# Optimization experiments

Measured on AMD Instinct MI355X. Metric: run time of the kernel, lower is better.

Reference implementation:

```python
import jax, jax.numpy as jnp
import numpy as np


def setup_inputs() -> dict:
    B, N, D, M = 512, 128, 768, 32  # bags, num_class, embed_dim, max bag size
    rng = np.random.default_rng(0)
    sizes = rng.integers(8, 25, size=B)  # variable bag sizes in [8, 24], all <= M
    offsets = np.concatenate([[0], np.cumsum(sizes)]).astype(np.int32)
    nsum = int(offsets[-1])
    scope = np.stack([offsets[:-1], offsets[1:]], axis=1)  # (B, 2) [start, end)

    key = jax.random.key(0)
    k1, k2, k3 = jax.random.split(key, 3)
    rep = jax.random.normal(k1, (nsum, D), dtype=jnp.float32)
    fc_weight = jax.random.normal(k2, (N, D), dtype=jnp.float32) * 0.02
    fc_bias = jax.random.normal(k3, (N,), dtype=jnp.float32) * 0.02
    return {
        "rep": rep,
        "fc_weight": fc_weight,
        "fc_bias": fc_bias,
        "scope": jnp.asarray(scope),
        "max_bag": M,
    }


def reference(rep, fc_weight, fc_bias, scope, max_bag):
    """IntraBagAttention forward (train=False, bag_size=0 branch), ragged bags
    rewritten as padded/masked dense ops.

    rep:       (nsum, D) sentence-encoder outputs
    fc_weight: (N, D), fc_bias: (N,)
    scope:     (B, 2) int [start, end) per bag; max_bag: static int pad bound
    returns:   (B, N) per-relation bag scores
    """
    nsum = rep.shape[0]
    starts = scope[:, 0]
    sizes = scope[:, 1] - scope[:, 0]
    pos = jnp.arange(max_bag)
    idx = jnp.clip(starts[:, None] + pos[None, :], 0, nsum - 1)  # (B, M)
    valid = pos[None, :] < sizes[:, None]                        # (B, M)
    bag = rep[idx]                                               # (B, M, D)

    # att_score = rep @ fc.weight.data.T ; .data => no grad through this use
    w_att = jax.lax.stop_gradient(fc_weight)
    att = jnp.einsum('bmd,nd->bnm', bag, w_att)                  # (B, N, M)
    att = jnp.where(valid[:, None, :], att, -jnp.inf)
    sm = jax.nn.softmax(att, axis=-1)                            # per-bag softmax over sentences

    # weighted segment sum: one attended rep per relation per bag
    rfer = jnp.einsum('bnm,bmd->bnd', sm, bag)                   # (B, N, D)

    # fc(rep_for_each_rel) -> (B, N, N); softmax over classes; take diagonal
    full = jnp.einsum('bnd,kd->bnk', rfer, fc_weight) + fc_bias  # (B, N, N)
    probs = jax.nn.softmax(full, axis=-1)
    return jnp.diagonal(probs, axis1=1, axis2=2)                 # (B, N)
```

## Files before the change

### kernel.cpp

```cpp
#include <hip/hip_runtime.h>
#include <math.h>

#define B_BAGS 512
#define N_REL  128
#define D_DIM  768

typedef __attribute__((ext_vector_type(8))) short  bf16x8;
typedef __attribute__((ext_vector_type(4))) float  f32x4;

__device__ inline unsigned pack_hi(float f0, float f1) {
    return __builtin_amdgcn_perm(__float_as_uint(f1), __float_as_uint(f0), 0x07060302u);
}
__device__ inline float trunc_res(float f) {
    return f - __uint_as_float(__float_as_uint(f) & 0xFFFF0000u);
}

__global__ void build_bfrag(const float* __restrict__ W, unsigned* __restrict__ Bfrag) {
    int flat = blockIdx.x * 256 + threadIdx.x;
    int lane = flat & 63;
    int tile = (flat >> 6) & 7;
    int s    = flat >> 9;
    int n  = tile * 16 + (lane & 15);
    int k0 = s * 32 + (lane >> 4) * 8;
    const float* src = &W[n * D_DIM + k0];
    float f[8];
    #pragma unroll
    for (int j = 0; j < 8; ++j) f[j] = src[j];
    unsigned hi[4], lo[4];
    #pragma unroll
    for (int q = 0; q < 4; ++q) {
        hi[q] = pack_hi(f[2*q], f[2*q+1]);
        lo[q] = pack_hi(trunc_res(f[2*q]), trunc_res(f[2*q+1]));
    }
    unsigned base = (unsigned)(((s * 8 + tile) * 2) * 64 + lane) * 4;
    *(uint4*)&Bfrag[base]          = make_uint4(hi[0], hi[1], hi[2], hi[3]);
    *(uint4*)&Bfrag[base + 64 * 4] = make_uint4(lo[0], lo[1], lo[2], lo[3]);
}

__global__ __launch_bounds__(512, 4) void bag_fused(
    const float*          __restrict__ rep,
    const unsigned short* __restrict__ Bfrag,
    const float*          __restrict__ bias,
    const int*            __restrict__ scope,
    float*                __restrict__ out,
    int nsum)
{
    __shared__ f32x4    Gpart[2][2][8][64];
    __shared__ unsigned Gfrag[8 * 2 * 64 * 4];
    __shared__ unsigned SMfrag[8 * 2 * 64 * 4];

    const int t = threadIdx.x;
    const int b = blockIdx.x;
    const int start = scope[2 * b];
    const int size  = scope[2 * b + 1] - start;

    const int wv   = t >> 6;
    const int lane = t & 63;
    const int nl15 = lane & 15;
    const int lg   = lane >> 4;
    const int h    = wv >> 2;
    const int q    = wv & 3;

    const float* rpA[2];
    #pragma unroll
    for (int mt = 0; mt < 2; ++mt) {
        int row = start + mt * 16 + nl15;
        row = (row > nsum - 1) ? (nsum - 1) : row;
        rpA[mt] = &rep[(size_t)row * D_DIM + h * 384 + lg * 8];
    }

    f32x4 acc[2][2][2];
    #pragma unroll
    for (int mt = 0; mt < 2; ++mt)
        #pragma unroll
        for (int ntl = 0; ntl < 2; ++ntl) {
            acc[mt][ntl][0] = f32x4{0.f, 0.f, 0.f, 0.f};
            acc[mt][ntl][1] = f32x4{0.f, 0.f, 0.f, 0.f};
        }

    float4 cr[2][2];
    uint4  cbh[2], cbl[2];
    #pragma unroll
    for (int mt = 0; mt < 2; ++mt) {
        cr[mt][0] = *(const float4*)&rpA[mt][0];
        cr[mt][1] = *(const float4*)&rpA[mt][4];
    }
    #pragma unroll
    for (int ntl = 0; ntl < 2; ++ntl) {
        const int tid8 = (h * 12) * 8 + q * 2 + ntl;
        cbh[ntl] = *(const uint4*)&Bfrag[((size_t)(tid8 * 2 + 0) * 64 + lane) * 8];
        cbl[ntl] = *(const uint4*)&Bfrag[((size_t)(tid8 * 2 + 1) * 64 + lane) * 8];
    }

    #pragma unroll
    for (int s = 0; s < 12; ++s) {
        float4 nr[2][2];
        uint4  nbh[2], nbl[2];
        if (s < 11) {
            #pragma unroll
            for (int mt = 0; mt < 2; ++mt) {
                nr[mt][0] = *(const float4*)&rpA[mt][(s + 1) * 32];
                nr[mt][1] = *(const float4*)&rpA[mt][(s + 1) * 32 + 4];
            }
            #pragma unroll
            for (int ntl = 0; ntl < 2; ++ntl) {
                const int tid8 = (h * 12 + s + 1) * 8 + q * 2 + ntl;
                nbh[ntl] = *(const uint4*)&Bfrag[((size_t)(tid8 * 2 + 0) * 64 + lane) * 8];
                nbl[ntl] = *(const uint4*)&Bfrag[((size_t)(tid8 * 2 + 1) * 64 + lane) * 8];
            }
        }

        union { unsigned u[4]; bf16x8 v; } ah[2], al[2];
        #pragma unroll
        for (int mt = 0; mt < 2; ++mt) {
            const float4 v0 = cr[mt][0];
            const float4 v1 = cr[mt][1];
            ah[mt].u[0] = pack_hi(v0.x, v0.y);
            ah[mt].u[1] = pack_hi(v0.z, v0.w);
            ah[mt].u[2] = pack_hi(v1.x, v1.y);
            ah[mt].u[3] = pack_hi(v1.z, v1.w);
            al[mt].u[0] = pack_hi(trunc_res(v0.x), trunc_res(v0.y));
            al[mt].u[1] = pack_hi(trunc_res(v0.z), trunc_res(v0.w));
            al[mt].u[2] = pack_hi(trunc_res(v1.x), trunc_res(v1.y));
            al[mt].u[3] = pack_hi(trunc_res(v1.z), trunc_res(v1.w));
        }
        #pragma unroll
        for (int ntl = 0; ntl < 2; ++ntl) {
            union { uint4 u; bf16x8 v; } bh, bl;
            bh.u = cbh[ntl];
            bl.u = cbl[ntl];
            #pragma unroll
            for (int mt = 0; mt < 2; ++mt) {
                acc[mt][ntl][0] = __builtin_amdgcn_mfma_f32_16x16x32_bf16(ah[mt].v, bh.v, acc[mt][ntl][0], 0, 0, 0);
                acc[mt][ntl][1] = __builtin_amdgcn_mfma_f32_16x16x32_bf16(ah[mt].v, bl.v, acc[mt][ntl][1], 0, 0, 0);
                acc[mt][ntl][1] = __builtin_amdgcn_mfma_f32_16x16x32_bf16(al[mt].v, bh.v, acc[mt][ntl][1], 0, 0, 0);
            }
        }

        if (s < 11) {
            #pragma unroll
            for (int mt = 0; mt < 2; ++mt) { cr[mt][0] = nr[mt][0]; cr[mt][1] = nr[mt][1]; }
            #pragma unroll
            for (int ntl = 0; ntl < 2; ++ntl) { cbh[ntl] = nbh[ntl]; cbl[ntl] = nbl[ntl]; }
        }
    }

    #pragma unroll
    for (int mt = 0; mt < 2; ++mt)
        #pragma unroll
        for (int ntl = 0; ntl < 2; ++ntl)
            Gpart[h][mt][q * 2 + ntl][lane] = acc[mt][ntl][0] + acc[mt][ntl][1];
    __syncthreads();

    const int T = wv;
    float gv[2][4], smv[2][4];
    #pragma unroll
    for (int mt = 0; mt < 2; ++mt) {
        const f32x4 p0 = Gpart[0][mt][T][lane];
        const f32x4 p1 = Gpart[1][mt][T][lane];
        #pragma unroll
        for (int r = 0; r < 4; ++r) gv[mt][r] = p0[r] + p1[r];
    }

    float vmax = -INFINITY;
    #pragma unroll
    for (int mt = 0; mt < 2; ++mt)
        #pragma unroll
        for (int r = 0; r < 4; ++r) {
            const int m = mt * 16 + lg * 4 + r;
            if (m < size) vmax = fmaxf(vmax, gv[mt][r]);
        }
    vmax = fmaxf(vmax, __shfl_xor(vmax, 16));
    vmax = fmaxf(vmax, __shfl_xor(vmax, 32));

    float ssum = 0.f;
    #pragma unroll
    for (int mt = 0; mt < 2; ++mt)
        #pragma unroll
        for (int r = 0; r < 4; ++r) {
            const int m = mt * 16 + lg * 4 + r;
            float e = (m < size) ? __expf(gv[mt][r] - vmax) : 0.f;
            smv[mt][r] = e;
            ssum += e;
        }
    ssum += __shfl_xor(ssum, 16);
    ssum += __shfl_xor(ssum, 32);
    const float inv = 1.f / ssum;
    #pragma unroll
    for (int mt = 0; mt < 2; ++mt)
        #pragma unroll
        for (int r = 0; r < 4; ++r) smv[mt][r] *= inv;

    #pragma unroll
    for (int mt = 0; mt < 2; ++mt)
        #pragma unroll
        for (int rp = 0; rp < 4; rp += 2) {
            const int m     = mt * 16 + lg * 4 + rp;
            const int lane2 = (m >> 3) * 16 + nl15;
            const int word  = (m >> 1) & 3;
            const int ihi = ((T * 2 + 0) * 64 + lane2) * 4 + word;
            const int ilo = ((T * 2 + 1) * 64 + lane2) * 4 + word;
            Gfrag[ihi]  = pack_hi(gv[mt][rp], gv[mt][rp + 1]);
            Gfrag[ilo]  = pack_hi(trunc_res(gv[mt][rp]), trunc_res(gv[mt][rp + 1]));
            SMfrag[ihi] = pack_hi(smv[mt][rp], smv[mt][rp + 1]);
            SMfrag[ilo] = pack_hi(trunc_res(smv[mt][rp]), trunc_res(smv[mt][rp + 1]));
        }
    __syncthreads();

    float bias_r[8];
    #pragma unroll
    for (int ct = 0; ct < 8; ++ct) bias_r[ct] = bias[ct * 16 + nl15];

    f32x4 facc[8];
    #pragma unroll
    for (int ct = 0; ct < 8; ++ct) facc[ct] = f32x4{0.f, 0.f, 0.f, 0.f};

    const bf16x8 ah2 = *(const bf16x8*)&SMfrag[((T * 2 + 0) * 64 + lane) * 4];
    const bf16x8 al2 = *(const bf16x8*)&SMfrag[((T * 2 + 1) * 64 + lane) * 4];
    #pragma unroll
    for (int ct = 0; ct < 8; ++ct) {
        const bf16x8 bh = *(const bf16x8*)&Gfrag[((ct * 2 + 0) * 64 + lane) * 4];
        const bf16x8 bl = *(const bf16x8*)&Gfrag[((ct * 2 + 1) * 64 + lane) * 4];
        facc[ct] = __builtin_amdgcn_mfma_f32_16x16x32_bf16(ah2, bh, facc[ct], 0, 0, 0);
        facc[ct] = __builtin_amdgcn_mfma_f32_16x16x32_bf16(ah2, bl, facc[ct], 0, 0, 0);
        facc[ct] = __builtin_amdgcn_mfma_f32_16x16x32_bf16(al2, bh, facc[ct], 0, 0, 0);
    }

    #pragma unroll
    for (int r = 0; r < 4; ++r) {
        float s[8];
        #pragma unroll
        for (int ct = 0; ct < 8; ++ct) s[ct] = facc[ct][r] + bias_r[ct];

        float mx = s[0];
        #pragma unroll
        for (int ct = 1; ct < 8; ++ct) mx = fmaxf(mx, s[ct]);
        mx = fmaxf(mx, __shfl_xor(mx, 1));
        mx = fmaxf(mx, __shfl_xor(mx, 2));
        mx = fmaxf(mx, __shfl_xor(mx, 4));
        mx = fmaxf(mx, __shfl_xor(mx, 8));

        float l = 0.f;
        #pragma unroll
        for (int ct = 0; ct < 8; ++ct) l += __expf(s[ct] - mx);
        l += __shfl_xor(l, 1);
        l += __shfl_xor(l, 2);
        l += __shfl_xor(l, 4);
        l += __shfl_xor(l, 8);

        const int nl = lg * 4 + r;
        float sd = s[0];
        #pragma unroll
        for (int ct = 1; ct < 8; ++ct) sd = (ct == T) ? s[ct] : sd;
        if (nl15 == nl) {
            out[b * N_REL + T * 16 + nl] = __expf(sd - mx) / l;
        }
    }
}

extern "C" void kernel_launch(void* const* d_in, const int* in_sizes, int n_in,
                              void* d_out, int out_size, void* d_ws, size_t ws_size,
                              hipStream_t stream) {
    const float* rep   = (const float*)d_in[0];
    const float* W     = (const float*)d_in[1];
    const float* bias  = (const float*)d_in[2];
    const int*   scope = (const int*)d_in[3];

    const int nsum = in_sizes[0] / D_DIM;
    unsigned* Bfrag = (unsigned*)d_ws;

    build_bfrag<<<48, 256, 0, stream>>>(W, Bfrag);
    bag_fused<<<B_BAGS, 512, 0, stream>>>(rep, (const unsigned short*)Bfrag,
                                          bias, scope, (float*)d_out, nsum);
}
```

Baseline: 104.1 us.

## Precompute bf16 hi/lo A fragments of rep in a separate prep kernel

Adds an afrag_prep kernel that splits every rep row once into packed bf16 high and residual-low fragments, laid out in 16-row groups in workspace. The fused bag kernel then loads ready-made A and B fragments directly instead of converting fp32 rep in its inner loop, and drops the manual register prefetch double-buffering. The aim is to remove the duplicated per-block conversion work for overlapping padded windows. In exchange it adds a kernel launch and an extra full write and read of the converted rep through global memory.

New measurement: 103.3 us. Within noise of the previous version (-0.8%).

```diff
diff --git a/kernel.cpp b/kernel.cpp
--- a/kernel.cpp
+++ b/kernel.cpp
@@ -13,6 +13,26 @@
 }
 __device__ inline float trunc_res(float f) {
     return f - __uint_as_float(__float_as_uint(f) & 0xFFFF0000u);
+}
+
+__global__ void afrag_prep(const float* __restrict__ rep,
+                           unsigned* __restrict__ Afrag, int nsum) {
+    const int grp = blockIdx.x;
+    const int t   = threadIdx.x;
+    #pragma unroll
+    for (int i = 0; i < 24; ++i) {
+        const int u   = i * 256 + t;
+        const int gs  = u >> 8;
+        const int rem = u & 255;
+        const int r   = rem >> 4;
+        const int jw  = rem & 15;
+        int row = grp * 16 + r;
+        row = (row > nsum - 1) ? (nsum - 1) : row;
+        const float2 f = *(const float2*)&rep[(size_t)row * D_DIM + gs * 32 + jw * 2];
+        const unsigned base = (unsigned)((grp * 24 + gs) * 2) * 256 + rem;
+        Afrag[base]       = pack_hi(f.x, f.y);
+        Afrag[base + 256] = pack_hi(trunc_res(f.x), trunc_res(f.y));
+    }
 }
 
 __global__ void build_bfrag(const float* __restrict__ W, unsigned* __restrict__ Bfrag) {
@@ -38,11 +58,11 @@
 }
 
 __global__ __launch_bounds__(512, 4) void bag_fused(
-    const float*          __restrict__ rep,
-    const unsigned short* __restrict__ Bfrag,
-    const float*          __restrict__ bias,
-    const int*            __restrict__ scope,
-    float*                __restrict__ out,
+    const unsigned* __restrict__ Afrag,
+    const unsigned* __restrict__ Bfrag,
+    const float*    __restrict__ bias,
+    const int*      __restrict__ scope,
+    float*          __restrict__ out,
     int nsum)
 {
     __shared__ f32x4    Gpart[2][2][8][64];
@@ -61,13 +81,23 @@
     const int h    = wv >> 2;
     const int q    = wv & 3;
 
-    const float* rpA[2];
+    unsigned abase[2][2];
     #pragma unroll
     for (int mt = 0; mt < 2; ++mt) {
         int row = start + mt * 16 + nl15;
         row = (row > nsum - 1) ? (nsum - 1) : row;
-        rpA[mt] = &rep[(size_t)row * D_DIM + h * 384 + lg * 8];
-    }
+        const unsigned grp = (unsigned)row >> 4;
+        const unsigned r   = (unsigned)row & 15;
+        #pragma unroll
+        for (int p = 0; p < 2; ++p)
+            abase[mt][p] = ((grp * 24 + h * 12) * 2 + p) * 256 + r * 16 + lg * 4;
+    }
+    unsigned bbase[2][2];
+    #pragma unroll
+    for (int ntl = 0; ntl < 2; ++ntl)
+        #pragma unroll
+        for (int p = 0; p < 2; ++p)
+            bbase[ntl][p] = (((h * 12) * 8 + q * 2 + ntl) * 2 + p) * 256 + lane * 4;
 
     f32x4 acc[2][2][2];
     #pragma unroll
@@ -78,71 +108,27 @@
             acc[mt][ntl][1] = f32x4{0.f, 0.f, 0.f, 0.f};
         }
 
-    float4 cr[2][2];
-    uint4  cbh[2], cbl[2];
-    #pragma unroll
-    for (int mt = 0; mt < 2; ++mt) {
-        cr[mt][0] = *(const float4*)&rpA[mt][0];
-        cr[mt][1] = *(const float4*)&rpA[mt][4];
-    }
-    #pragma unroll
-    for (int ntl = 0; ntl < 2; ++ntl) {
-        const int tid8 = (h * 12) * 8 + q * 2 + ntl;
-        cbh[ntl] = *(const uint4*)&Bfrag[((size_t)(tid8 * 2 + 0) * 64 + lane) * 8];
-        cbl[ntl] = *(const uint4*)&Bfrag[((size_t)(tid8 * 2 + 1) * 64 + lane) * 8];
-    }
-
     #pragma unroll
     for (int s = 0; s < 12; ++s) {
-        float4 nr[2][2];
-        uint4  nbh[2], nbl[2];
-        if (s < 11) {
+        bf16x8 ah[2], al[2], bh[2], bl[2];
+        #pragma unroll
+        for (int mt = 0; mt < 2; ++mt) {
+            ah[mt] = *(const bf16x8*)&Afrag[abase[mt][0] + s * 512];
+            al[mt] = *(const bf16x8*)&Afrag[abase[mt][1] + s * 512];
+        }
+        #pragma unroll
+        for (int ntl = 0; ntl < 2; ++ntl) {
+            bh[ntl] = *(const bf16x8*)&Bfrag[bbase[ntl][0] + s * 4096];
+            bl[ntl] = *(const bf16x8*)&Bfrag[bbase[ntl][1] + s * 4096];
+        }
+        #pragma unroll
+        for (int ntl = 0; ntl < 2; ++ntl)
             #pragma unroll
             for (int mt = 0; mt < 2; ++mt) {
-                nr[mt][0] = *(const float4*)&rpA[mt][(s + 1) * 32];
-                nr[mt][1] = *(const float4*)&rpA[mt][(s + 1) * 32 + 4];
+                acc[mt][ntl][0] = __builtin_amdgcn_mfma_f32_16x16x32_bf16(ah[mt], bh[ntl], acc[mt][ntl][0], 0, 0, 0);
+                acc[mt][ntl][1] = __builtin_amdgcn_mfma_f32_16x16x32_bf16(ah[mt], bl[ntl], acc[mt][ntl][1], 0, 0, 0);
+                acc[mt][ntl][1] = __builtin_amdgcn_mfma_f32_16x16x32_bf16(al[mt], bh[ntl], acc[mt][ntl][1], 0, 0, 0);
             }
-            #pragma unroll
-            for (int ntl = 0; ntl < 2; ++ntl) {
-                const int tid8 = (h * 12 + s + 1) * 8 + q * 2 + ntl;
-                nbh[ntl] = *(const uint4*)&Bfrag[((size_t)(tid8 * 2 + 0) * 64 + lane) * 8];
-                nbl[ntl] = *(const uint4*)&Bfrag[((size_t)(tid8 * 2 + 1) * 64 + lane) * 8];
-            }
-        }
-
-        union { unsigned u[4]; bf16x8 v; } ah[2], al[2];
-        #pragma unroll
-        for (int mt = 0; mt < 2; ++mt) {
-            const float4 v0 = cr[mt][0];
-            const float4 v1 = cr[mt][1];
-            ah[mt].u[0] = pack_hi(v0.x, v0.y);
-            ah[mt].u[1] = pack_hi(v0.z, v0.w);
-            ah[mt].u[2] = pack_hi(v1.x, v1.y);
-            ah[mt].u[3] = pack_hi(v1.z, v1.w);
-            al[mt].u[0] = pack_hi(trunc_res(v0.x), trunc_res(v0.y));
-            al[mt].u[1] = pack_hi(trunc_res(v0.z), trunc_res(v0.w));
-            al[mt].u[2] = pack_hi(trunc_res(v1.x), trunc_res(v1.y));
-            al[mt].u[3] = pack_hi(trunc_res(v1.z), trunc_res(v1.w));
-        }
-        #pragma unroll
-        for (int ntl = 0; ntl < 2; ++ntl) {
-            union { uint4 u; bf16x8 v; } bh, bl;
-            bh.u = cbh[ntl];
-            bl.u = cbl[ntl];
-            #pragma unroll
-            for (int mt = 0; mt < 2; ++mt) {
-                acc[mt][ntl][0] = __builtin_amdgcn_mfma_f32_16x16x32_bf16(ah[mt].v, bh.v, acc[mt][ntl][0], 0, 0, 0);
-                acc[mt][ntl][1] = __builtin_amdgcn_mfma_f32_16x16x32_bf16(ah[mt].v, bl.v, acc[mt][ntl][1], 0, 0, 0);
-                acc[mt][ntl][1] = __builtin_amdgcn_mfma_f32_16x16x32_bf16(al[mt].v, bh.v, acc[mt][ntl][1], 0, 0, 0);
-            }
-        }
-
-        if (s < 11) {
-            #pragma unroll
-            for (int mt = 0; mt < 2; ++mt) { cr[mt][0] = nr[mt][0]; cr[mt][1] = nr[mt][1]; }
-            #pragma unroll
-            for (int ntl = 0; ntl < 2; ++ntl) { cbh[ntl] = nbh[ntl]; cbl[ntl] = nbl[ntl]; }
-        }
     }
 
     #pragma unroll
@@ -266,10 +252,14 @@
     const float* bias  = (const float*)d_in[2];
     const int*   scope = (const int*)d_in[3];
 
-    const int nsum = in_sizes[0] / D_DIM;
+    const int nsum   = in_sizes[0] / D_DIM;
+    const int groups = (nsum + 15) >> 4;
+
     unsigned* Bfrag = (unsigned*)d_ws;
+    unsigned* Afrag = (unsigned*)((char*)d_ws + 393216);
 
     build_bfrag<<<48, 256, 0, stream>>>(W, Bfrag);
-    bag_fused<<<B_BAGS, 512, 0, stream>>>(rep, (const unsigned short*)Bfrag,
-                                          bias, scope, (float*)d_out, nsum);
-}
+    afrag_prep<<<groups, 256, 0, stream>>>(rep, Afrag, nsum);
+    bag_fused<<<B_BAGS, 512, 0, stream>>>(Afrag, Bfrag, bias, scope,
+                                          (float*)d_out, nsum);
+}
```
